# Optimization experiments

Measured on AMD Instinct MI355X. Metric: run time of the kernel, lower is better.

The kernel has to match this reference:

```python
import jax, jax.numpy as jnp
import numpy as np

N_USERS = 100000
M_ITEMS = 50000
N = N_USERS + M_ITEMS
D = 64
NNZ = 4800000
N_LAYERS = 3


def spmm(idx, val, x):
    # sparse COO (idx[0]=rows, idx[1]=cols) @ dense x : gather-scale-scatter
    rows, cols = idx[0], idx[1]
    return jax.ops.segment_sum(val[:, None] * x[cols], rows, num_segments=N)


def propagate(idx, val, emb0):
    # LightGCN propagation: mean over layer-0..n_layers embeddings
    embs = [emb0]
    e = emb0
    for _ in range(N_LAYERS):
        e = spmm(idx, val, e)
        embs.append(e)
    return jnp.mean(jnp.stack(embs, axis=1), axis=1)  # [N, D]


def setup_inputs() -> dict:
    key = jax.random.key(0)
    ks = jax.random.split(key, 10)
    return {
        "emb_im": 0.1 * jax.random.normal(ks[0], (N, D), jnp.float32),
        "emb_q": 0.1 * jax.random.normal(ks[1], (N, D), jnp.float32),
        "emb_p": 0.1 * jax.random.normal(ks[2], (N, D), jnp.float32),
        "g_im_idx": jax.random.randint(ks[3], (2, NNZ), 0, N, jnp.int32),
        "g_im_val": jax.random.uniform(ks[4], (NNZ,), jnp.float32) / 32.0,
        "g_q_idx": jax.random.randint(ks[5], (2, NNZ), 0, N, jnp.int32),
        "g_q_val": jax.random.uniform(ks[6], (NNZ,), jnp.float32) / 32.0,
        "g_p_idx": jax.random.randint(ks[7], (2, NNZ), 0, N, jnp.int32),
        "g_p_val": jax.random.uniform(ks[8], (NNZ,), jnp.float32) / 32.0,
        "add_weight": jnp.ones((3,), jnp.float32),
    }


def reference(emb_im, emb_q, emb_p, g_im_idx, g_im_val, g_q_idx, g_q_val,
              g_p_idx, g_p_val, add_weight):
    out_im = propagate(g_im_idx, g_im_val, emb_im)
    out_q = propagate(g_q_idx, g_q_val, emb_q)
    out_p = propagate(g_p_idx, g_p_val, emb_p)
    # weighted_add over factors: sum_f w_f * out_f ; users/items split is a
    # row split of this combined [N, D] matrix
    stacked = jnp.stack([out_im, out_q, out_p], axis=0)  # [3, N, D]
    combined = jnp.sum(stacked * add_weight[:, None, None], axis=0)  # [N, D]
    return combined  # rows [:N_USERS] = users, rows [N_USERS:] = items
```

## Files before the change

kernel.cpp:

```cpp
#include <hip/hip_runtime.h>

#define N_TOTAL 150000
#define DIM 64
#define RPB 293
#define NBUCK 512
#define MAGIC 14658592u
#define CAP 10368
#define CHUNK 8192

typedef float v2f __attribute__((ext_vector_type(2)));

__global__ void fill_bcur_kernel(int* __restrict__ bcur) {
    int t = blockIdx.x * 256 + threadIdx.x;
    if (t < NBUCK) bcur[t] = t * CAP;
}

__global__ void bin_kernel(const int* __restrict__ idx, const float* __restrict__ val,
                           int* __restrict__ bcur, uint2* __restrict__ binned, int nnz) {
    __shared__ uint2 sedge[CHUNK];
    __shared__ int lcnt[NBUCK];
    __shared__ int lstart[NBUCK + 1];
    __shared__ int gbase[NBUCK];
    int t = threadIdx.x;
    int base = blockIdx.x * CHUNK;
    int nEdges = min(CHUNK, nnz - base);
    lcnt[t] = 0;
    __syncthreads();
    uint2 myedge[16];
    int myb[16];
    #pragma unroll
    for (int i = 0; i < 16; ++i) {
        int e = base + t + i * 512;
        if (e < nnz) {
            int r = idx[e];
            int b = (int)__umulhi((unsigned)r, MAGIC);
            myb[i] = b;
            unsigned rloc = (unsigned)(r - b * RPB);
            myedge[i].x = (rloc << 18) | (unsigned)idx[nnz + e];
            myedge[i].y = __float_as_uint(val[e]);
            atomicAdd(&lcnt[b], 1);
        } else {
            myb[i] = -1;
        }
    }
    __syncthreads();
    int c = lcnt[t];
    lstart[t] = c;
    __syncthreads();
    for (int off = 1; off < 512; off <<= 1) {
        int x = (t >= off) ? lstart[t - off] : 0;
        __syncthreads();
        lstart[t] += x;
        __syncthreads();
    }
    int incl = lstart[t];
    __syncthreads();
    lstart[t] = incl - c;
    if (t == 511) lstart[512] = incl;
    gbase[t] = c ? atomicAdd(&bcur[t], c) : 0;
    lcnt[t] = 0;
    __syncthreads();
    #pragma unroll
    for (int i = 0; i < 16; ++i) {
        int b = myb[i];
        if (b >= 0) {
            int o = atomicAdd(&lcnt[b], 1);
            sedge[lstart[b] + o] = myedge[i];
        }
    }
    __syncthreads();
    for (int p = t; p < nEdges; p += 512) {
        int lo = 0, hi = NBUCK;
        while (hi - lo > 1) {
            int mid = (lo + hi) >> 1;
            if (lstart[mid] <= p) lo = mid; else hi = mid;
        }
        int dst = gbase[lo] + (p - lstart[lo]);
        if (dst < (lo + 1) * CAP)
            binned[dst] = sedge[p];
    }
}

__global__ void scatterc_kernel(const uint2* __restrict__ binned,
                                const int* __restrict__ bcur,
                                int* __restrict__ rlo, int* __restrict__ rhi,
                                unsigned* __restrict__ cs) {
    __shared__ int hist[RPB];
    __shared__ int ssc[256];
    int b = blockIdx.x, t = threadIdx.x;
    int s = b * CAP, e = min(bcur[b], s + CAP);
    for (int i = t; i < RPB; i += 256) hist[i] = 0;
    __syncthreads();
    for (int k = s + t; k < e; k += 256)
        atomicAdd(&hist[binned[k].x >> 18], 1);
    __syncthreads();
    int i0 = 2 * t;
    int c0 = (i0 < RPB) ? hist[i0] : 0;
    int c1 = (i0 + 1 < RPB) ? hist[i0 + 1] : 0;
    int s2 = c0 + c1;
    ssc[t] = s2;
    __syncthreads();
    for (int off = 1; off < 256; off <<= 1) {
        int x = (t >= off) ? ssc[t - off] : 0;
        __syncthreads();
        ssc[t] += x;
        __syncthreads();
    }
    int excl = ssc[t] - s2;
    __syncthreads();
    int base0 = s + excl, base1 = s + excl + c0;
    if (i0 < RPB) {
        int row = b * RPB + i0;
        if (row < N_TOTAL) { rlo[row] = base0; rhi[row] = base0 + c0; }
        hist[i0] = base0;
    }
    if (i0 + 1 < RPB) {
        int row = b * RPB + i0 + 1;
        if (row < N_TOTAL) { rlo[row] = base1; rhi[row] = base1 + c1; }
        hist[i0 + 1] = base1;
    }
    __syncthreads();
    for (int k = s + t; k < e; k += 256) {
        uint2 ed = binned[k];
        int rl_ = ed.x >> 18;
        int o = atomicAdd(&hist[rl_], 1);
        unsigned v14 = (ed.y + 0x20000u) >> 18;
        cs[o] = ((ed.x & 0x3FFFFu) << 14) | v14;
    }
}

__global__ void conv_fp8_kernel(const float* __restrict__ x, uint2* __restrict__ y, int n8) {
    int i = blockIdx.x * blockDim.x + threadIdx.x;
    if (i >= n8) return;
    const float4* x4 = reinterpret_cast<const float4*>(x);
    float4 a = x4[2 * i], b = x4[2 * i + 1];
    int p0 = __builtin_amdgcn_cvt_pk_fp8_f32(a.x * 64.f, a.y * 64.f, 0, false);
    p0 = __builtin_amdgcn_cvt_pk_fp8_f32(a.z * 64.f, a.w * 64.f, p0, true);
    int p1 = __builtin_amdgcn_cvt_pk_fp8_f32(b.x * 64.f, b.y * 64.f, 0, false);
    p1 = __builtin_amdgcn_cvt_pk_fp8_f32(b.z * 64.f, b.w * 64.f, p1, true);
    uint2 o;
    o.x = (unsigned)p0;
    o.y = (unsigned)p1;
    y[i] = o;
}

__global__ void spmm_fp8_kernel(const int* __restrict__ rlo, const int* __restrict__ rhi,
                                const unsigned* __restrict__ cs, const unsigned* __restrict__ x,
                                unsigned* __restrict__ y, int nrows) {
    int gid = blockIdx.x * blockDim.x + threadIdx.x;
    int row = gid >> 6;
    int lane = gid & 63;
    if (row >= nrows) return;
    int s = rlo[row], e = rhi[row];
    int q = lane >> 4, sub = lane & 15;
    float ac[4][4];
    #pragma unroll
    for (int j = 0; j < 4; ++j) {
        ac[j][0] = 0.f; ac[j][1] = 0.f; ac[j][2] = 0.f; ac[j][3] = 0.f;
    }
    int k = s + q;
    for (; k + 12 < e; k += 16) {
        unsigned ed[4], g[4];
        #pragma unroll
        for (int j = 0; j < 4; ++j) ed[j] = cs[k + 4 * j];
        #pragma unroll
        for (int j = 0; j < 4; ++j) g[j] = x[((size_t)(ed[j] >> 14) << 4) + sub];
        #pragma unroll
        for (int j = 0; j < 4; ++j) {
            float vv = __uint_as_float((ed[j] & 0x3FFFu) << 18);
            v2f lo = __builtin_amdgcn_cvt_pk_f32_fp8((int)g[j], false);
            v2f hi = __builtin_amdgcn_cvt_pk_f32_fp8((int)g[j], true);
            ac[j][0] += vv * lo.x;
            ac[j][1] += vv * lo.y;
            ac[j][2] += vv * hi.x;
            ac[j][3] += vv * hi.y;
        }
    }
    for (; k < e; k += 4) {
        unsigned ed = cs[k];
        unsigned g = x[((size_t)(ed >> 14) << 4) + sub];
        float vv = __uint_as_float((ed & 0x3FFFu) << 18);
        v2f lo = __builtin_amdgcn_cvt_pk_f32_fp8((int)g, false);
        v2f hi = __builtin_amdgcn_cvt_pk_f32_fp8((int)g, true);
        ac[0][0] += vv * lo.x;
        ac[0][1] += vv * lo.y;
        ac[0][2] += vv * hi.x;
        ac[0][3] += vv * hi.y;
    }
    float a0 = (ac[0][0] + ac[1][0]) + (ac[2][0] + ac[3][0]);
    float a1 = (ac[0][1] + ac[1][1]) + (ac[2][1] + ac[3][1]);
    float a2 = (ac[0][2] + ac[1][2]) + (ac[2][2] + ac[3][2]);
    float a3 = (ac[0][3] + ac[1][3]) + (ac[2][3] + ac[3][3]);
    a0 += __shfl_xor(a0, 16); a0 += __shfl_xor(a0, 32);
    a1 += __shfl_xor(a1, 16); a1 += __shfl_xor(a1, 32);
    a2 += __shfl_xor(a2, 16); a2 += __shfl_xor(a2, 32);
    a3 += __shfl_xor(a3, 16); a3 += __shfl_xor(a3, 32);
    if (q == 0) {
        int p = __builtin_amdgcn_cvt_pk_fp8_f32(a0, a1, 0, false);
        p = __builtin_amdgcn_cvt_pk_fp8_f32(a2, a3, p, true);
        y[((size_t)row << 4) + sub] = (unsigned)p;
    }
}

template <bool FIRST>
__global__ void combine_kernel(const float* __restrict__ emb, const unsigned* __restrict__ A,
                               const unsigned* __restrict__ B, const unsigned* __restrict__ C,
                               const float* __restrict__ w, int f, float* __restrict__ out,
                               int nwords) {
    int i = blockIdx.x * blockDim.x + threadIdx.x;
    if (i >= nwords) return;
    float c = w[f] * 0.25f;
    const float kInv = 1.f / 64.f;
    float4 e = reinterpret_cast<const float4*>(emb)[i];
    unsigned a = A[i], b = B[i], cc = C[i];
    v2f alo = __builtin_amdgcn_cvt_pk_f32_fp8((int)a, false);
    v2f ahi = __builtin_amdgcn_cvt_pk_f32_fp8((int)a, true);
    v2f blo = __builtin_amdgcn_cvt_pk_f32_fp8((int)b, false);
    v2f bhi = __builtin_amdgcn_cvt_pk_f32_fp8((int)b, true);
    v2f clo = __builtin_amdgcn_cvt_pk_f32_fp8((int)cc, false);
    v2f chi = __builtin_amdgcn_cvt_pk_f32_fp8((int)cc, true);
    float4 o;
    o.x = c * (e.x + (alo.x + blo.x + clo.x) * kInv);
    o.y = c * (e.y + (alo.y + blo.y + clo.y) * kInv);
    o.z = c * (e.z + (ahi.x + bhi.x + chi.x) * kInv);
    o.w = c * (e.w + (ahi.y + bhi.y + chi.y) * kInv);
    float4* o4 = reinterpret_cast<float4*>(out) + i;
    if (FIRST) {
        *o4 = o;
    } else {
        float4 cv = *o4;
        cv.x += o.x; cv.y += o.y; cv.z += o.z; cv.w += o.w;
        *o4 = cv;
    }
}

extern "C" void kernel_launch(void* const* d_in, const int* in_sizes, int n_in,
                              void* d_out, int out_size, void* d_ws, size_t ws_size,
                              hipStream_t stream) {
    const float* emb[3]  = {(const float*)d_in[0], (const float*)d_in[1], (const float*)d_in[2]};
    const int*   gidx[3] = {(const int*)d_in[3],   (const int*)d_in[5],   (const int*)d_in[7]};
    const float* gval[3] = {(const float*)d_in[4], (const float*)d_in[6], (const float*)d_in[8]};
    const float* w = (const float*)d_in[9];
    float* out = (float*)d_out;

    const int nnz = in_sizes[4];
    const size_t bufElems = (size_t)N_TOTAL * DIM;
    const size_t fp8Bytes = bufElems;
    const size_t capElems = (size_t)NBUCK * CAP;

    char* base = (char*)d_ws;
    uint2*    binned = (uint2*)base;
    unsigned* emb8   = (unsigned*)base;
    unsigned* A8     = (unsigned*)(base + fp8Bytes);
    unsigned* B8     = (unsigned*)(base + 2 * fp8Bytes);
    unsigned* C8     = (unsigned*)(base + 3 * fp8Bytes);
    unsigned* cs     = (unsigned*)(base + capElems * 8);
    int*      rlo    = (int*)(base + capElems * 8 + capElems * 4);
    int*      rhi    = rlo + N_TOTAL;
    int*      bcur   = rhi + N_TOTAL;

    const int n8 = (int)(bufElems / 8);
    const int nwords = (int)(bufElems / 4);
    dim3 cvtGrid((n8 + 255) / 256);
    dim3 cmbGrid((nwords + 255) / 256);
    dim3 chunkGrid((nnz + CHUNK - 1) / CHUNK);
    dim3 rowGrid((unsigned)(((size_t)N_TOTAL * 64 + 255) / 256));

    for (int f = 0; f < 3; ++f) {
        fill_bcur_kernel<<<2, 256, 0, stream>>>(bcur);
        bin_kernel<<<chunkGrid, 512, 0, stream>>>(gidx[f], gval[f], bcur, binned, nnz);
        scatterc_kernel<<<NBUCK, 256, 0, stream>>>(binned, bcur, rlo, rhi, cs);

        conv_fp8_kernel<<<cvtGrid, 256, 0, stream>>>(emb[f], (uint2*)emb8, n8);

        spmm_fp8_kernel<<<rowGrid, 256, 0, stream>>>(rlo, rhi, cs, emb8, A8, N_TOTAL);
        spmm_fp8_kernel<<<rowGrid, 256, 0, stream>>>(rlo, rhi, cs, A8, B8, N_TOTAL);
        spmm_fp8_kernel<<<rowGrid, 256, 0, stream>>>(rlo, rhi, cs, B8, C8, N_TOTAL);

        if (f == 0)
            combine_kernel<true><<<cmbGrid, 256, 0, stream>>>(emb[f], A8, B8, C8, w, f,
                                                              out, nwords);
        else
            combine_kernel<false><<<cmbGrid, 256, 0, stream>>>(emb[f], A8, B8, C8, w, f,
                                                               out, nwords);
    }
}
```

Baseline: 1.093 ms.

## Split binned edges into packed cs and short row, widen SpMM lanes, fuse combine

The binning pass now writes the final packed column/value word plus a 16-bit local row in place of an 8-byte edge record. This cuts binned-buffer traffic, and recomputing the bucket from the row replaces the per-edge binary search. The SpMM kernel now has each lane load 8 fp8 values (uint2) across 8 lanes per edge, with 8 edges in flight per row and two accumulator sets. When workspace allows, the three per-factor combine passes are replaced by a single combine over all nine layer tables, which needs more workspace.

```diff
diff --git a/kernel.cpp b/kernel.cpp
--- a/kernel.cpp
+++ b/kernel.cpp
@@ -16,8 +16,10 @@
 }
 
 __global__ void bin_kernel(const int* __restrict__ idx, const float* __restrict__ val,
-                           int* __restrict__ bcur, uint2* __restrict__ binned, int nnz) {
-    __shared__ uint2 sedge[CHUNK];
+                           int* __restrict__ bcur, unsigned* __restrict__ bcs,
+                           unsigned short* __restrict__ brl, int nnz) {
+    __shared__ unsigned scs[CHUNK];
+    __shared__ unsigned srow[CHUNK];
     __shared__ int lcnt[NBUCK];
     __shared__ int lstart[NBUCK + 1];
     __shared__ int gbase[NBUCK];
@@ -26,8 +28,8 @@
     int nEdges = min(CHUNK, nnz - base);
     lcnt[t] = 0;
     __syncthreads();
-    uint2 myedge[16];
-    int myb[16];
+    unsigned mycs[16];
+    int myrow[16], myb[16];
     #pragma unroll
     for (int i = 0; i < 16; ++i) {
         int e = base + t + i * 512;
@@ -35,9 +37,9 @@
             int r = idx[e];
             int b = (int)__umulhi((unsigned)r, MAGIC);
             myb[i] = b;
-            unsigned rloc = (unsigned)(r - b * RPB);
-            myedge[i].x = (rloc << 18) | (unsigned)idx[nnz + e];
-            myedge[i].y = __float_as_uint(val[e]);
+            myrow[i] = r;
+            unsigned v14 = (__float_as_uint(val[e]) + 0x20000u) >> 18;
+            mycs[i] = ((unsigned)idx[nnz + e] << 14) | v14;
             atomicAdd(&lcnt[b], 1);
         } else {
             myb[i] = -1;
@@ -65,23 +67,25 @@
         int b = myb[i];
         if (b >= 0) {
             int o = atomicAdd(&lcnt[b], 1);
-            sedge[lstart[b] + o] = myedge[i];
+            int p = lstart[b] + o;
+            scs[p] = mycs[i];
+            srow[p] = (unsigned)myrow[i];
         }
     }
     __syncthreads();
     for (int p = t; p < nEdges; p += 512) {
-        int lo = 0, hi = NBUCK;
-        while (hi - lo > 1) {
-            int mid = (lo + hi) >> 1;
-            if (lstart[mid] <= p) lo = mid; else hi = mid;
+        int r = (int)srow[p];
+        int b = (int)__umulhi((unsigned)r, MAGIC);
+        int dst = gbase[b] + (p - lstart[b]);
+        if (dst < (b + 1) * CAP) {
+            bcs[dst] = scs[p];
+            brl[dst] = (unsigned short)(r - b * RPB);
         }
-        int dst = gbase[lo] + (p - lstart[lo]);
-        if (dst < (lo + 1) * CAP)
-            binned[dst] = sedge[p];
-    }
-}
-
-__global__ void scatterc_kernel(const uint2* __restrict__ binned,
+    }
+}
+
+__global__ void scatterc_kernel(const unsigned* __restrict__ bcs,
+                                const unsigned short* __restrict__ brl,
                                 const int* __restrict__ bcur,
                                 int* __restrict__ rlo, int* __restrict__ rhi,
                                 unsigned* __restrict__ cs) {
@@ -92,7 +96,7 @@
     for (int i = t; i < RPB; i += 256) hist[i] = 0;
     __syncthreads();
     for (int k = s + t; k < e; k += 256)
-        atomicAdd(&hist[binned[k].x >> 18], 1);
+        atomicAdd(&hist[brl[k]], 1);
     __syncthreads();
     int i0 = 2 * t;
     int c0 = (i0 < RPB) ? hist[i0] : 0;
@@ -121,11 +125,9 @@
     }
     __syncthreads();
     for (int k = s + t; k < e; k += 256) {
-        uint2 ed = binned[k];
-        int rl_ = ed.x >> 18;
+        int rl_ = brl[k];
         int o = atomicAdd(&hist[rl_], 1);
-        unsigned v14 = (ed.y + 0x20000u) >> 18;
-        cs[o] = ((ed.x & 0x3FFFFu) << 14) | v14;
+        cs[o] = bcs[k];
     }
 }
 
@@ -145,66 +147,109 @@
 }
 
 __global__ void spmm_fp8_kernel(const int* __restrict__ rlo, const int* __restrict__ rhi,
-                                const unsigned* __restrict__ cs, const unsigned* __restrict__ x,
-                                unsigned* __restrict__ y, int nrows) {
+                                const unsigned* __restrict__ cs, const uint2* __restrict__ x2,
+                                uint2* __restrict__ y2, int nrows) {
     int gid = blockIdx.x * blockDim.x + threadIdx.x;
     int row = gid >> 6;
     int lane = gid & 63;
     if (row >= nrows) return;
     int s = rlo[row], e = rhi[row];
-    int q = lane >> 4, sub = lane & 15;
-    float ac[4][4];
+    int q = lane >> 3, sub = lane & 7;
+    float ac[8], bc[8];
     #pragma unroll
-    for (int j = 0; j < 4; ++j) {
-        ac[j][0] = 0.f; ac[j][1] = 0.f; ac[j][2] = 0.f; ac[j][3] = 0.f;
-    }
+    for (int d = 0; d < 8; ++d) { ac[d] = 0.f; bc[d] = 0.f; }
     int k = s + q;
-    for (; k + 12 < e; k += 16) {
-        unsigned ed[4], g[4];
-        #pragma unroll
-        for (int j = 0; j < 4; ++j) ed[j] = cs[k + 4 * j];
-        #pragma unroll
-        for (int j = 0; j < 4; ++j) g[j] = x[((size_t)(ed[j] >> 14) << 4) + sub];
-        #pragma unroll
-        for (int j = 0; j < 4; ++j) {
-            float vv = __uint_as_float((ed[j] & 0x3FFFu) << 18);
-            v2f lo = __builtin_amdgcn_cvt_pk_f32_fp8((int)g[j], false);
-            v2f hi = __builtin_amdgcn_cvt_pk_f32_fp8((int)g[j], true);
-            ac[j][0] += vv * lo.x;
-            ac[j][1] += vv * lo.y;
-            ac[j][2] += vv * hi.x;
-            ac[j][3] += vv * hi.y;
-        }
-    }
-    for (; k < e; k += 4) {
+    for (; k + 8 < e; k += 16) {
+        unsigned ed0 = cs[k], ed1 = cs[k + 8];
+        uint2 g0 = x2[((size_t)(ed0 >> 14) << 3) + sub];
+        uint2 g1 = x2[((size_t)(ed1 >> 14) << 3) + sub];
+        float v0 = __uint_as_float((ed0 & 0x3FFFu) << 18);
+        float v1 = __uint_as_float((ed1 & 0x3FFFu) << 18);
+        v2f l0 = __builtin_amdgcn_cvt_pk_f32_fp8((int)g0.x, false);
+        v2f h0 = __builtin_amdgcn_cvt_pk_f32_fp8((int)g0.x, true);
+        v2f l1 = __builtin_amdgcn_cvt_pk_f32_fp8((int)g0.y, false);
+        v2f h1 = __builtin_amdgcn_cvt_pk_f32_fp8((int)g0.y, true);
+        ac[0] += v0 * l0.x; ac[1] += v0 * l0.y; ac[2] += v0 * h0.x; ac[3] += v0 * h0.y;
+        ac[4] += v0 * l1.x; ac[5] += v0 * l1.y; ac[6] += v0 * h1.x; ac[7] += v0 * h1.y;
+        v2f l2 = __builtin_amdgcn_cvt_pk_f32_fp8((int)g1.x, false);
+        v2f h2 = __builtin_amdgcn_cvt_pk_f32_fp8((int)g1.x, true);
+        v2f l3 = __builtin_amdgcn_cvt_pk_f32_fp8((int)g1.y, false);
+        v2f h3 = __builtin_amdgcn_cvt_pk_f32_fp8((int)g1.y, true);
+        bc[0] += v1 * l2.x; bc[1] += v1 * l2.y; bc[2] += v1 * h2.x; bc[3] += v1 * h2.y;
+        bc[4] += v1 * l3.x; bc[5] += v1 * l3.y; bc[6] += v1 * h3.x; bc[7] += v1 * h3.y;
+    }
+    for (; k < e; k += 8) {
         unsigned ed = cs[k];
-        unsigned g = x[((size_t)(ed >> 14) << 4) + sub];
+        uint2 g = x2[((size_t)(ed >> 14) << 3) + sub];
         float vv = __uint_as_float((ed & 0x3FFFu) << 18);
-        v2f lo = __builtin_amdgcn_cvt_pk_f32_fp8((int)g, false);
-        v2f hi = __builtin_amdgcn_cvt_pk_f32_fp8((int)g, true);
-        ac[0][0] += vv * lo.x;
-        ac[0][1] += vv * lo.y;
-        ac[0][2] += vv * hi.x;
-        ac[0][3] += vv * hi.y;
-    }
-    float a0 = (ac[0][0] + ac[1][0]) + (ac[2][0] + ac[3][0]);
-    float a1 = (ac[0][1] + ac[1][1]) + (ac[2][1] + ac[3][1]);
-    float a2 = (ac[0][2] + ac[1][2]) + (ac[2][2] + ac[3][2]);
-    float a3 = (ac[0][3] + ac[1][3]) + (ac[2][3] + ac[3][3]);
-    a0 += __shfl_xor(a0, 16); a0 += __shfl_xor(a0, 32);
-    a1 += __shfl_xor(a1, 16); a1 += __shfl_xor(a1, 32);
-    a2 += __shfl_xor(a2, 16); a2 += __shfl_xor(a2, 32);
-    a3 += __shfl_xor(a3, 16); a3 += __shfl_xor(a3, 32);
+        v2f l0 = __builtin_amdgcn_cvt_pk_f32_fp8((int)g.x, false);
+        v2f h0 = __builtin_amdgcn_cvt_pk_f32_fp8((int)g.x, true);
+        v2f l1 = __builtin_amdgcn_cvt_pk_f32_fp8((int)g.y, false);
+        v2f h1 = __builtin_amdgcn_cvt_pk_f32_fp8((int)g.y, true);
+        ac[0] += vv * l0.x; ac[1] += vv * l0.y; ac[2] += vv * h0.x; ac[3] += vv * h0.y;
+        ac[4] += vv * l1.x; ac[5] += vv * l1.y; ac[6] += vv * h1.x; ac[7] += vv * h1.y;
+    }
+    #pragma unroll
+    for (int d = 0; d < 8; ++d) {
+        float a = ac[d] + bc[d];
+        a += __shfl_xor(a, 8);
+        a += __shfl_xor(a, 16);
+        a += __shfl_xor(a, 32);
+        ac[d] = a;
+    }
     if (q == 0) {
-        int p = __builtin_amdgcn_cvt_pk_fp8_f32(a0, a1, 0, false);
-        p = __builtin_amdgcn_cvt_pk_fp8_f32(a2, a3, p, true);
-        y[((size_t)row << 4) + sub] = (unsigned)p;
-    }
+        int p0 = __builtin_amdgcn_cvt_pk_fp8_f32(ac[0], ac[1], 0, false);
+        p0 = __builtin_amdgcn_cvt_pk_fp8_f32(ac[2], ac[3], p0, true);
+        int p1 = __builtin_amdgcn_cvt_pk_fp8_f32(ac[4], ac[5], 0, false);
+        p1 = __builtin_amdgcn_cvt_pk_fp8_f32(ac[6], ac[7], p1, true);
+        uint2 o;
+        o.x = (unsigned)p0;
+        o.y = (unsigned)p1;
+        y2[((size_t)row << 3) + sub] = o;
+    }
+}
+
+__device__ inline float4 dec_sum3(const unsigned* __restrict__ T, int i, int nwords) {
+    unsigned a = T[i], b = T[i + nwords], c = T[i + 2 * nwords];
+    v2f alo = __builtin_amdgcn_cvt_pk_f32_fp8((int)a, false);
+    v2f ahi = __builtin_amdgcn_cvt_pk_f32_fp8((int)a, true);
+    v2f blo = __builtin_amdgcn_cvt_pk_f32_fp8((int)b, false);
+    v2f bhi = __builtin_amdgcn_cvt_pk_f32_fp8((int)b, true);
+    v2f clo = __builtin_amdgcn_cvt_pk_f32_fp8((int)c, false);
+    v2f chi = __builtin_amdgcn_cvt_pk_f32_fp8((int)c, true);
+    float4 r;
+    r.x = alo.x + blo.x + clo.x;
+    r.y = alo.y + blo.y + clo.y;
+    r.z = ahi.x + bhi.x + chi.x;
+    r.w = ahi.y + bhi.y + chi.y;
+    return r;
+}
+
+__global__ void combine3_kernel(const float* __restrict__ e0, const float* __restrict__ e1,
+                                const float* __restrict__ e2, const unsigned* __restrict__ t0,
+                                const unsigned* __restrict__ t1, const unsigned* __restrict__ t2,
+                                const float* __restrict__ w, float* __restrict__ out,
+                                int nwords) {
+    int i = blockIdx.x * blockDim.x + threadIdx.x;
+    if (i >= nwords) return;
+    const float kInv = 1.f / 64.f;
+    float c0 = w[0] * 0.25f, c1 = w[1] * 0.25f, c2 = w[2] * 0.25f;
+    float4 ev0 = reinterpret_cast<const float4*>(e0)[i];
+    float4 ev1 = reinterpret_cast<const float4*>(e1)[i];
+    float4 ev2 = reinterpret_cast<const float4*>(e2)[i];
+    float4 s0 = dec_sum3(t0, i, nwords);
+    float4 s1 = dec_sum3(t1, i, nwords);
+    float4 s2 = dec_sum3(t2, i, nwords);
+    float4 o;
+    o.x = c0 * (ev0.x + kInv * s0.x) + c1 * (ev1.x + kInv * s1.x) + c2 * (ev2.x + kInv * s2.x);
+    o.y = c0 * (ev0.y + kInv * s0.y) + c1 * (ev1.y + kInv * s1.y) + c2 * (ev2.y + kInv * s2.y);
+    o.z = c0 * (ev0.z + kInv * s0.z) + c1 * (ev1.z + kInv * s1.z) + c2 * (ev2.z + kInv * s2.z);
+    o.w = c0 * (ev0.w + kInv * s0.w) + c1 * (ev1.w + kInv * s1.w) + c2 * (ev2.w + kInv * s2.w);
+    reinterpret_cast<float4*>(out)[i] = o;
 }
 
 template <bool FIRST>
-__global__ void combine_kernel(const float* __restrict__ emb, const unsigned* __restrict__ A,
-                               const unsigned* __restrict__ B, const unsigned* __restrict__ C,
+__global__ void combine_kernel(const float* __restrict__ emb, const unsigned* __restrict__ T,
                                const float* __restrict__ w, int f, float* __restrict__ out,
                                int nwords) {
     int i = blockIdx.x * blockDim.x + threadIdx.x;
@@ -212,18 +257,12 @@
     float c = w[f] * 0.25f;
     const float kInv = 1.f / 64.f;
     float4 e = reinterpret_cast<const float4*>(emb)[i];
-    unsigned a = A[i], b = B[i], cc = C[i];
-    v2f alo = __builtin_amdgcn_cvt_pk_f32_fp8((int)a, false);
-    v2f ahi = __builtin_amdgcn_cvt_pk_f32_fp8((int)a, true);
-    v2f blo = __builtin_amdgcn_cvt_pk_f32_fp8((int)b, false);
-    v2f bhi = __builtin_amdgcn_cvt_pk_f32_fp8((int)b, true);
-    v2f clo = __builtin_amdgcn_cvt_pk_f32_fp8((int)cc, false);
-    v2f chi = __builtin_amdgcn_cvt_pk_f32_fp8((int)cc, true);
+    float4 s = dec_sum3(T, i, nwords);
     float4 o;
-    o.x = c * (e.x + (alo.x + blo.x + clo.x) * kInv);
-    o.y = c * (e.y + (alo.y + blo.y + clo.y) * kInv);
-    o.z = c * (e.z + (ahi.x + bhi.x + chi.x) * kInv);
-    o.w = c * (e.w + (ahi.y + bhi.y + chi.y) * kInv);
+    o.x = c * (e.x + s.x * kInv);
+    o.y = c * (e.y + s.y * kInv);
+    o.z = c * (e.z + s.z * kInv);
+    o.w = c * (e.w + s.w * kInv);
     float4* o4 = reinterpret_cast<float4*>(out) + i;
     if (FIRST) {
         *o4 = o;
@@ -249,15 +288,16 @@
     const size_t capElems = (size_t)NBUCK * CAP;
 
     char* base = (char*)d_ws;
-    uint2*    binned = (uint2*)base;
-    unsigned* emb8   = (unsigned*)base;
-    unsigned* A8     = (unsigned*)(base + fp8Bytes);
-    unsigned* B8     = (unsigned*)(base + 2 * fp8Bytes);
-    unsigned* C8     = (unsigned*)(base + 3 * fp8Bytes);
-    unsigned* cs     = (unsigned*)(base + capElems * 8);
-    int*      rlo    = (int*)(base + capElems * 8 + capElems * 4);
-    int*      rhi    = rlo + N_TOTAL;
-    int*      bcur   = rhi + N_TOTAL;
+    unsigned*       bcs  = (unsigned*)base;
+    unsigned*       emb8 = (unsigned*)base;
+    unsigned short* brl  = (unsigned short*)(base + capElems * 4);
+    unsigned*       cs   = (unsigned*)(base + capElems * 6);
+    int*            rlo  = (int*)(base + capElems * 10);
+    int*            rhi  = rlo + N_TOTAL;
+    int*            bcur = rhi + N_TOTAL;
+    char*           tab  = base + capElems * 10 + (size_t)2 * N_TOTAL * 4 + 4096;
+    const size_t needFused = (tab - base) + (size_t)9 * fp8Bytes;
+    const bool fused = ws_size >= needFused;
 
     const int n8 = (int)(bufElems / 8);
     const int nwords = (int)(bufElems / 4);
@@ -267,21 +307,36 @@
     dim3 rowGrid((unsigned)(((size_t)N_TOTAL * 64 + 255) / 256));
 
     for (int f = 0; f < 3; ++f) {
+        unsigned* A8 = (unsigned*)(tab + (size_t)(fused ? 3 * f + 0 : 0) * fp8Bytes);
+        unsigned* B8 = (unsigned*)(tab + (size_t)(fused ? 3 * f + 1 : 1) * fp8Bytes);
+        unsigned* C8 = (unsigned*)(tab + (size_t)(fused ? 3 * f + 2 : 2) * fp8Bytes);
+
         fill_bcur_kernel<<<2, 256, 0, stream>>>(bcur);
-        bin_kernel<<<chunkGrid, 512, 0, stream>>>(gidx[f], gval[f], bcur, binned, nnz);
-        scatterc_kernel<<<NBUCK, 256, 0, stream>>>(binned, bcur, rlo, rhi, cs);
+        bin_kernel<<<chunkGrid, 512, 0, stream>>>(gidx[f], gval[f], bcur, bcs, brl, nnz);
+        scatterc_kernel<<<NBUCK, 256, 0, stream>>>(bcs, brl, bcur, rlo, rhi, cs);
 
         conv_fp8_kernel<<<cvtGrid, 256, 0, stream>>>(emb[f], (uint2*)emb8, n8);
 
-        spmm_fp8_kernel<<<rowGrid, 256, 0, stream>>>(rlo, rhi, cs, emb8, A8, N_TOTAL);
-        spmm_fp8_kernel<<<rowGrid, 256, 0, stream>>>(rlo, rhi, cs, A8, B8, N_TOTAL);
-        spmm_fp8_kernel<<<rowGrid, 256, 0, stream>>>(rlo, rhi, cs, B8, C8, N_TOTAL);
-
-        if (f == 0)
-            combine_kernel<true><<<cmbGrid, 256, 0, stream>>>(emb[f], A8, B8, C8, w, f,
-                                                              out, nwords);
-        else
-            combine_kernel<false><<<cmbGrid, 256, 0, stream>>>(emb[f], A8, B8, C8, w, f,
-                                                               out, nwords);
-    }
-}
+        spmm_fp8_kernel<<<rowGrid, 256, 0, stream>>>(rlo, rhi, cs, (const uint2*)emb8,
+                                                     (uint2*)A8, N_TOTAL);
+        spmm_fp8_kernel<<<rowGrid, 256, 0, stream>>>(rlo, rhi, cs, (const uint2*)A8,
+                                                     (uint2*)B8, N_TOTAL);
+        spmm_fp8_kernel<<<rowGrid, 256, 0, stream>>>(rlo, rhi, cs, (const uint2*)B8,
+                                                     (uint2*)C8, N_TOTAL);
+
+        if (!fused) {
+            if (f == 0)
+                combine_kernel<true><<<cmbGrid, 256, 0, stream>>>(emb[f], A8, w, f, out, nwords);
+            else
+                combine_kernel<false><<<cmbGrid, 256, 0, stream>>>(emb[f], A8, w, f, out, nwords);
+        }
+    }
+
+    if (fused) {
+        const unsigned* t0 = (const unsigned*)(tab + (size_t)0 * fp8Bytes);
+        const unsigned* t1 = (const unsigned*)(tab + (size_t)3 * fp8Bytes);
+        const unsigned* t2 = (const unsigned*)(tab + (size_t)6 * fp8Bytes);
+        combine3_kernel<<<cmbGrid, 256, 0, stream>>>(emb[0], emb[1], emb[2], t0, t1, t2,
+                                                     w, out, nwords);
+    }
+}
```

Measured after the change: 986.9 us. -9.7%, faster.
